# Kernel optimization log

Hardware: AMD Instinct MI355X
Metric: run time of the kernel (lower is better)

The kernel has to match this reference:

```python
import jax, jax.numpy as jnp
import numpy as np

NUM_COMPONENTS = 4
HEADS = 16

def setup_inputs() -> dict:
    key = jax.random.key(0)
    ks = jax.random.split(key, 7)
    BC, S, D = 8, 4096, 1024   # batch*components, latent tokens, hidden dim
    E = 160                     # encoder (text) sequence length
    w_scale = 0.02              # keep logits in a sane range
    return {
        "hidden_states": jax.random.normal(ks[0], (BC, S, D), jnp.float32),
        "encoder_hidden_states": jax.random.normal(ks[1], (BC, E, D), jnp.float32),
        "Wq": jax.random.normal(ks[2], (D, D), jnp.float32) * w_scale,
        "Wk": jax.random.normal(ks[3], (D, D), jnp.float32) * w_scale,
        "Wv": jax.random.normal(ks[4], (D, D), jnp.float32) * w_scale,
        "Wo": jax.random.normal(ks[5], (D, D), jnp.float32) * w_scale,
        "bo": jnp.zeros((D,), jnp.float32),
    }

def reference(hidden_states, encoder_hidden_states, Wq, Wk, Wv, Wo, bo):
    BC, S, D = hidden_states.shape
    E = encoder_hidden_states.shape[1]
    C = NUM_COMPONENTS
    B = BC // C
    H = HEADS
    dh = D // H
    scale = dh ** -0.5

    # projections (diffusers to_q/to_k/to_v, no bias)
    q = hidden_states @ Wq            # [BC, S, D]
    k = encoder_hidden_states @ Wk    # [BC, E, D]
    v = encoder_hidden_states @ Wv    # [BC, E, D]

    q = q.reshape(BC, S, H, dh).transpose(0, 2, 1, 3)  # [BC, H, S, dh]
    k = k.reshape(BC, E, H, dh).transpose(0, 2, 1, 3)  # [BC, H, E, dh]
    v = v.reshape(BC, E, H, dh).transpose(0, 2, 1, 3)  # [BC, H, E, dh]

    scores = jnp.einsum("bhsd,bhtd->bhst", q, k) * scale  # [BC, H, S, E]
    scores_c = scores.reshape(C, B, H, S, E)

    # pooled (mean over encoder tokens) softmax across components
    pooled = scores_c.mean(axis=-1, keepdims=True)         # [C, B, H, S, 1]
    weights_pooled = jax.nn.softmax(pooled, axis=0)        # softmax over components
    # per-row softmax over encoder tokens, scaled by component weight
    weights = jax.nn.softmax(scores_c, axis=-1) * weights_pooled
    weights = weights.reshape(BC, H, S, E)

    out = jnp.einsum("bhst,bhtd->bhsd", weights, v)        # [BC, H, S, dh]
    out = out.transpose(0, 2, 1, 3).reshape(BC, S, D)

    out = out @ Wo + bo        # to_out[0]; to_out[1] is dropout (identity, eval)
    out = out + hidden_states  # residual_connection=True, rescale factor 1
    return out
```

## Files before the change

### kernel.cpp

```cpp
#include <hip/hip_runtime.h>
#include <stdint.h>

typedef __attribute__((ext_vector_type(8))) short short8;
typedef __attribute__((ext_vector_type(4))) float f32x4;
typedef __attribute__((ext_vector_type(4))) unsigned short us4;

#define DI __device__ __forceinline__

static constexpr int Dm = 1024;
static constexpr int Sm = 4096;
static constexpr int Em = 160;
static constexpr int Hm = 16;

static constexpr size_t OFF_HSB  = 0;
static constexpr size_t OFF_WT   = 67108864;
static constexpr size_t OFF_QB   = 75497472;
static constexpr size_t OFF_KB   = 142606336;
static constexpr size_t OFF_VB   = 145227776;
static constexpr size_t OFF_VT   = 147849216;
static constexpr size_t OFF_EHSB = 150994944;

DI unsigned short f2b(float f) {
  union { float f; unsigned u; } x; x.f = f;
  unsigned r = x.u + 0x7fffu + ((x.u >> 16) & 1u);
  return (unsigned short)(r >> 16);
}

DI void gl_lds16(const void* g, void* l) {
  __builtin_amdgcn_global_load_lds(
      (const __attribute__((address_space(1))) unsigned int*)g,
      (__attribute__((address_space(3))) unsigned int*)l, 16, 0, 0);
}

__global__ void k_cvt(const float* __restrict__ in, unsigned short* __restrict__ out, int n4) {
  int stride = gridDim.x * blockDim.x;
  for (int i = blockIdx.x * blockDim.x + threadIdx.x; i < n4; i += stride) {
    float4 v = ((const float4*)in)[i];
    us4 o = { f2b(v.x), f2b(v.y), f2b(v.z), f2b(v.w) };
    *(us4*)(out + (size_t)i * 4) = o;
  }
}

__global__ void k_wtrans(const float* __restrict__ W0, const float* __restrict__ W1,
                         const float* __restrict__ W2, const float* __restrict__ W3,
                         unsigned short* __restrict__ Wt) {
  __shared__ float t[32][33];
  const float* W = (blockIdx.z == 0) ? W0 : (blockIdx.z == 1) ? W1 : (blockIdx.z == 2) ? W2 : W3;
  unsigned short* o = Wt + (size_t)blockIdx.z * 1048576;
  int tx = threadIdx.x, ty = threadIdx.y;
  int n = blockIdx.x * 32 + tx;
  int k0 = blockIdx.y * 32;
  #pragma unroll
  for (int j = ty; j < 32; j += 8) t[j][tx] = W[(size_t)(k0 + j) * 1024 + n];
  __syncthreads();
  #pragma unroll
  for (int j = ty; j < 32; j += 8)
    o[(size_t)(blockIdx.x * 32 + j) * 1024 + k0 + tx] = f2b(t[tx][j]);
}

template<int MODE>
__global__ __launch_bounds__(256, 2) void k_gemm(const unsigned short* __restrict__ A,
                                                 const unsigned short* __restrict__ Bt,
                                                 void* __restrict__ Cout,
                                                 const float* __restrict__ bias,
                                                 const float* __restrict__ resid) {
  __shared__ __align__(16) char smem[32768];
  char* As = smem;
  char* Bs = smem + 16384;
  const int tid = threadIdx.x;
  const int lane = tid & 63;
  const int l15 = lane & 15;
  const int g = lane >> 4;
  const int wv = tid >> 6;
  const int wr = wv >> 1, wc = wv & 1;
  const int m0 = blockIdx.x * 128, n0 = blockIdx.y * 128;

  f32x4 acc[4][4];
  #pragma unroll
  for (int i = 0; i < 4; ++i)
    #pragma unroll
    for (int j = 0; j < 4; ++j) acc[i][j] = (f32x4){0.f, 0.f, 0.f, 0.f};

  for (int t = 0; t < 16; ++t) {
    __syncthreads();
    #pragma unroll
    for (int is = 0; is < 4; ++is) {
      int ch = is * 256 + tid;
      int row = ch >> 3, j = ch & 7;
      int sj = (j ^ (row & 7)) * 8;
      gl_lds16(A  + (size_t)(m0 + row) * 1024 + t * 64 + sj, As + ch * 16);
      gl_lds16(Bt + (size_t)(n0 + row) * 1024 + t * 64 + sj, Bs + ch * 16);
    }
    __syncthreads();
    short8 af[2][4], bf[2][4];
    #pragma unroll
    for (int kk = 0; kk < 2; ++kk)
      #pragma unroll
      for (int mt = 0; mt < 4; ++mt) {
        af[kk][mt] = *(const short8*)(As + (wr * 64 + mt * 16 + l15) * 128 + ((kk * 64 + g * 16) ^ ((l15 & 7) << 4)));
        bf[kk][mt] = *(const short8*)(Bs + (wc * 64 + mt * 16 + l15) * 128 + ((kk * 64 + g * 16) ^ ((l15 & 7) << 4)));
      }
    #pragma unroll
    for (int kk = 0; kk < 2; ++kk)
      #pragma unroll
      for (int mt = 0; mt < 4; ++mt)
        #pragma unroll
        for (int nt = 0; nt < 4; ++nt)
          acc[mt][nt] = __builtin_amdgcn_mfma_f32_16x16x32_bf16(af[kk][mt], bf[kk][nt], acc[mt][nt], 0, 0, 0);
  }

  #pragma unroll
  for (int mt = 0; mt < 4; ++mt)
    #pragma unroll
    for (int nt = 0; nt < 4; ++nt)
      #pragma unroll
      for (int r = 0; r < 4; ++r) {
        size_t row = (size_t)(m0 + wr * 64 + mt * 16 + 4 * g + r);
        int col = n0 + wc * 64 + nt * 16 + l15;
        size_t idx = row * 1024 + col;
        if (MODE == 0) ((unsigned short*)Cout)[idx] = f2b(acc[mt][nt][r]);
        else           ((float*)Cout)[idx] = acc[mt][nt][r] + bias[col] + resid[idx];
      }
}

__global__ __launch_bounds__(256, 2) void k_gemm_kv(const unsigned short* __restrict__ A,
                                                    const unsigned short* __restrict__ Wt,
                                                    unsigned short* __restrict__ kb,
                                                    unsigned short* __restrict__ vt) {
  __shared__ __align__(16) char smem[32768];
  char* As = smem;
  char* Bs = smem + 16384;
  const int tid = threadIdx.x;
  const int lane = tid & 63;
  const int l15 = lane & 15;
  const int g = lane >> 4;
  const int wv = tid >> 6;
  const int wr = wv >> 1, wc = wv & 1;
  const int m0 = blockIdx.x * 128, n0 = blockIdx.y * 128;
  const int z = blockIdx.z;
  const unsigned short* Bt = Wt + (size_t)(1 + z) * 1048576;

  f32x4 acc[4][4];
  #pragma unroll
  for (int i = 0; i < 4; ++i)
    #pragma unroll
    for (int j = 0; j < 4; ++j) acc[i][j] = (f32x4){0.f, 0.f, 0.f, 0.f};

  for (int t = 0; t < 16; ++t) {
    __syncthreads();
    #pragma unroll
    for (int is = 0; is < 4; ++is) {
      int ch = is * 256 + tid;
      int row = ch >> 3, j = ch & 7;
      int sj = (j ^ (row & 7)) * 8;
      gl_lds16(A  + (size_t)(m0 + row) * 1024 + t * 64 + sj, As + ch * 16);
      gl_lds16(Bt + (size_t)(n0 + row) * 1024 + t * 64 + sj, Bs + ch * 16);
    }
    __syncthreads();
    short8 af[2][4], bf[2][4];
    #pragma unroll
    for (int kk = 0; kk < 2; ++kk)
      #pragma unroll
      for (int mt = 0; mt < 4; ++mt) {
        af[kk][mt] = *(const short8*)(As + (wr * 64 + mt * 16 + l15) * 128 + ((kk * 64 + g * 16) ^ ((l15 & 7) << 4)));
        bf[kk][mt] = *(const short8*)(Bs + (wc * 64 + mt * 16 + l15) * 128 + ((kk * 64 + g * 16) ^ ((l15 & 7) << 4)));
      }
    #pragma unroll
    for (int kk = 0; kk < 2; ++kk)
      #pragma unroll
      for (int mt = 0; mt < 4; ++mt)
        #pragma unroll
        for (int nt = 0; nt < 4; ++nt)
          acc[mt][nt] = __builtin_amdgcn_mfma_f32_16x16x32_bf16(af[kk][mt], bf[kk][nt], acc[mt][nt], 0, 0, 0);
  }

  #pragma unroll
  for (int mt = 0; mt < 4; ++mt)
    #pragma unroll
    for (int nt = 0; nt < 4; ++nt)
      #pragma unroll
      for (int r = 0; r < 4; ++r) {
        int row = m0 + wr * 64 + mt * 16 + 4 * g + r;
        int col = n0 + wc * 64 + nt * 16 + l15;
        unsigned short hv = f2b(acc[mt][nt][r]);
        if (z == 0) {
          kb[(size_t)row * 1024 + col] = hv;
        } else {
          int bc = row / 160, e = row - bc * 160;
          vt[((size_t)(bc * 16 + (col >> 6)) * 64 + (col & 63)) * 192 + e] = hv;
        }
      }
}

__global__ __launch_bounds__(256, 2) void k_attn(const unsigned short* __restrict__ Qb,
                                                 const unsigned short* __restrict__ Kb,
                                                 const unsigned short* __restrict__ Vt,
                                                 unsigned short* __restrict__ AOb) {
  __shared__ __align__(16) char smem[22528];
  float* pooled = (float*)(smem + 21504);
  const int tid = threadIdx.x, lane = tid & 63, wv = tid >> 6;
  const int g = lane >> 4, l15 = lane & 15;
  const int s0 = blockIdx.x * 64;
  const int h = blockIdx.y;
  const int b = blockIdx.z;
  const int bc = wv * 2 + b;
  const float scale = 0.125f;

  const unsigned short* Qp = Qb + ((size_t)bc * Sm + s0) * Dm + h * 64;
  const unsigned short* Kp = Kb + (size_t)bc * Em * Dm + h * 64;
  const unsigned short* Vp = Vt + ((size_t)bc * Hm + h) * (64 * 192);
  unsigned short* Op = AOb + ((size_t)bc * Sm + s0) * Dm + h * 64;
  char* Pw = smem + wv * 5376;

  #pragma unroll 1
  for (int st = 0; st < 4; ++st) {
    short8 qf[2];
    #pragma unroll
    for (int kk = 0; kk < 2; ++kk)
      qf[kk] = *(const short8*)(Qp + (size_t)(st * 16 + l15) * Dm + kk * 32 + g * 8);
    f32x4 sc[10];
    #pragma unroll
    for (int et = 0; et < 10; ++et) {
      sc[et] = (f32x4){0.f, 0.f, 0.f, 0.f};
      #pragma unroll
      for (int kk = 0; kk < 2; ++kk) {
        short8 kf = *(const short8*)(Kp + (size_t)(et * 16 + l15) * Dm + kk * 32 + g * 8);
        sc[et] = __builtin_amdgcn_mfma_f32_16x16x32_bf16(qf[kk], kf, sc[et], 0, 0, 0);
      }
    }
    float rs4[4];
    #pragma unroll
    for (int r = 0; r < 4; ++r) {
      float v = 0.f;
      #pragma unroll
      for (int et = 0; et < 10; ++et) v += sc[et][r];
      v += __shfl_xor(v, 1); v += __shfl_xor(v, 2); v += __shfl_xor(v, 4); v += __shfl_xor(v, 8);
      if (l15 == 0) pooled[(st * 16 + 4 * g + r) * 4 + wv] = v * (scale / 160.f);
      float mx = sc[0][r];
      #pragma unroll
      for (int et = 1; et < 10; ++et) mx = fmaxf(mx, sc[et][r]);
      mx = fmaxf(mx, __shfl_xor(mx, 1)); mx = fmaxf(mx, __shfl_xor(mx, 2));
      mx = fmaxf(mx, __shfl_xor(mx, 4)); mx = fmaxf(mx, __shfl_xor(mx, 8));
      float rs = 0.f;
      #pragma unroll
      for (int et = 0; et < 10; ++et) {
        float p = __expf((sc[et][r] - mx) * scale);
        rs += p;
        *(unsigned short*)(Pw + (4 * g + r) * 336 + (et * 16 + l15) * 2) = f2b(p);
      }
      rs += __shfl_xor(rs, 1); rs += __shfl_xor(rs, 2); rs += __shfl_xor(rs, 4); rs += __shfl_xor(rs, 8);
      rs4[r] = rs;
    }
    f32x4 oa[4];
    #pragma unroll
    for (int dt = 0; dt < 4; ++dt) oa[dt] = (f32x4){0.f, 0.f, 0.f, 0.f};
    #pragma unroll
    for (int k5 = 0; k5 < 5; ++k5) {
      short8 pf = *(const short8*)(Pw + l15 * 336 + k5 * 64 + g * 16);
      #pragma unroll
      for (int dt = 0; dt < 4; ++dt) {
        short8 vf = *(const short8*)(Vp + (size_t)(dt * 16 + l15) * 192 + k5 * 32 + g * 8);
        oa[dt] = __builtin_amdgcn_mfma_f32_16x16x32_bf16(pf, vf, oa[dt], 0, 0, 0);
      }
    }
    __syncthreads();
    #pragma unroll
    for (int r = 0; r < 4; ++r) {
      float4 pl = *(const float4*)&pooled[(st * 16 + 4 * g + r) * 4];
      float m3 = fmaxf(fmaxf(pl.x, pl.y), fmaxf(pl.z, pl.w));
      float ssum = __expf(pl.x - m3) + __expf(pl.y - m3) + __expf(pl.z - m3) + __expf(pl.w - m3);
      float mine = (wv == 0) ? pl.x : (wv == 1) ? pl.y : (wv == 2) ? pl.z : pl.w;
      float srw = __expf(mine - m3) / (ssum * rs4[r]);
      #pragma unroll
      for (int dt = 0; dt < 4; ++dt)
        Op[(size_t)(st * 16 + 4 * g + r) * Dm + dt * 16 + l15] = f2b(oa[dt][r] * srw);
    }
  }
}

extern "C" void kernel_launch(void* const* d_in, const int* in_sizes, int n_in,
                              void* d_out, int out_size, void* d_ws, size_t ws_size,
                              hipStream_t stream) {
  const float* hs  = (const float*)d_in[0];
  const float* ehs = (const float*)d_in[1];
  const float* Wq  = (const float*)d_in[2];
  const float* Wk  = (const float*)d_in[3];
  const float* Wv  = (const float*)d_in[4];
  const float* Wo  = (const float*)d_in[5];
  const float* bo  = (const float*)d_in[6];
  char* ws = (char*)d_ws;
  unsigned short* hsb = (unsigned short*)(ws + OFF_HSB);
  unsigned short* wt  = (unsigned short*)(ws + OFF_WT);
  unsigned short* qb  = (unsigned short*)(ws + OFF_QB);
  unsigned short* kb  = (unsigned short*)(ws + OFF_KB);
  unsigned short* vt  = (unsigned short*)(ws + OFF_VT);
  unsigned short* eb  = (unsigned short*)(ws + OFF_EHSB);

  hipLaunchKernelGGL(k_cvt, dim3(2048), dim3(256), 0, stream, hs, hsb, 8 * 4096 * 1024 / 4);
  hipLaunchKernelGGL(k_cvt, dim3(1280), dim3(256), 0, stream, ehs, eb, 8 * 160 * 1024 / 4);
  hipLaunchKernelGGL(k_wtrans, dim3(32, 32, 4), dim3(32, 8), 0, stream, Wq, Wk, Wv, Wo, wt);
  hipLaunchKernelGGL((k_gemm<0>), dim3(256, 8), dim3(256), 0, stream, hsb, wt, (void*)qb,
                     (const float*)nullptr, (const float*)nullptr);
  hipLaunchKernelGGL(k_gemm_kv, dim3(10, 8, 2), dim3(256), 0, stream, eb, wt, kb, vt);
  hipLaunchKernelGGL(k_attn, dim3(64, 16, 2), dim3(256), 0, stream, qb, kb, vt, hsb);
  hipLaunchKernelGGL((k_gemm<1>), dim3(256, 8), dim3(256), 0, stream, hsb, wt + 3 * 1048576, d_out, bo, hs);
}
```

Measured before the change: 359.8 us.

## Fuse fp32-to-bf16 conversion of hidden states into Q GEMM and swizzle block order

Drops the standalone conversion kernel for the 128MB fp32 hidden states and converts A tiles to bf16 inside the Q projection GEMM, writing them to LDS with regular loads and stores. This removes a full write and reread of the bf16 copy. Both GEMMs also switch to a 1D grid with grouped tile ordering, so blocks that share B tiles and A rows run close together for better L2 reuse. The cost is synchronous fp32 loads and per-element conversion inside the GEMM mainloop instead of async global-to-LDS loads.

```diff
diff --git a/kernel.cpp b/kernel.cpp
--- a/kernel.cpp
+++ b/kernel.cpp
@@ -16,7 +16,6 @@
 static constexpr size_t OFF_WT   = 67108864;
 static constexpr size_t OFF_QB   = 75497472;
 static constexpr size_t OFF_KB   = 142606336;
-static constexpr size_t OFF_VB   = 145227776;
 static constexpr size_t OFF_VT   = 147849216;
 static constexpr size_t OFF_EHSB = 150994944;
 
@@ -58,8 +57,8 @@
     o[(size_t)(blockIdx.x * 32 + j) * 1024 + k0 + tx] = f2b(t[tx][j]);
 }
 
-template<int MODE>
-__global__ __launch_bounds__(256, 2) void k_gemm(const unsigned short* __restrict__ A,
+template<int MODE, int CVTA>
+__global__ __launch_bounds__(256, 2) void k_gemm(const void* __restrict__ Ain,
                                                  const unsigned short* __restrict__ Bt,
                                                  void* __restrict__ Cout,
                                                  const float* __restrict__ bias,
@@ -73,7 +72,9 @@
   const int g = lane >> 4;
   const int wv = tid >> 6;
   const int wr = wv >> 1, wc = wv & 1;
-  const int m0 = blockIdx.x * 128, n0 = blockIdx.y * 128;
+  const int bid = blockIdx.x;
+  const int m0 = ((bid >> 6) * 8 + (bid & 7)) * 128;
+  const int n0 = ((bid >> 3) & 7) * 128;
 
   f32x4 acc[4][4];
   #pragma unroll
@@ -88,8 +89,23 @@
       int ch = is * 256 + tid;
       int row = ch >> 3, j = ch & 7;
       int sj = (j ^ (row & 7)) * 8;
-      gl_lds16(A  + (size_t)(m0 + row) * 1024 + t * 64 + sj, As + ch * 16);
       gl_lds16(Bt + (size_t)(n0 + row) * 1024 + t * 64 + sj, Bs + ch * 16);
+      if constexpr (!CVTA)
+        gl_lds16((const unsigned short*)Ain + (size_t)(m0 + row) * 1024 + t * 64 + sj, As + ch * 16);
+    }
+    if constexpr (CVTA) {
+      #pragma unroll
+      for (int is = 0; is < 4; ++is) {
+        int ch = is * 256 + tid;
+        int row = ch >> 3, j = ch & 7;
+        int sj = (j ^ (row & 7)) * 8;
+        const float* src = (const float*)Ain + (size_t)(m0 + row) * 1024 + t * 64 + sj;
+        float4 v0 = *(const float4*)src;
+        float4 v1 = *(const float4*)(src + 4);
+        short8 o = { (short)f2b(v0.x), (short)f2b(v0.y), (short)f2b(v0.z), (short)f2b(v0.w),
+                     (short)f2b(v1.x), (short)f2b(v1.y), (short)f2b(v1.z), (short)f2b(v1.w) };
+        *(short8*)(As + ch * 16) = o;
+      }
     }
     __syncthreads();
     short8 af[2][4], bf[2][4];
@@ -296,12 +312,11 @@
   unsigned short* vt  = (unsigned short*)(ws + OFF_VT);
   unsigned short* eb  = (unsigned short*)(ws + OFF_EHSB);
 
-  hipLaunchKernelGGL(k_cvt, dim3(2048), dim3(256), 0, stream, hs, hsb, 8 * 4096 * 1024 / 4);
   hipLaunchKernelGGL(k_cvt, dim3(1280), dim3(256), 0, stream, ehs, eb, 8 * 160 * 1024 / 4);
   hipLaunchKernelGGL(k_wtrans, dim3(32, 32, 4), dim3(32, 8), 0, stream, Wq, Wk, Wv, Wo, wt);
-  hipLaunchKernelGGL((k_gemm<0>), dim3(256, 8), dim3(256), 0, stream, hsb, wt, (void*)qb,
+  hipLaunchKernelGGL((k_gemm<0, 1>), dim3(2048), dim3(256), 0, stream, (const void*)hs, wt, (void*)qb,
                      (const float*)nullptr, (const float*)nullptr);
   hipLaunchKernelGGL(k_gemm_kv, dim3(10, 8, 2), dim3(256), 0, stream, eb, wt, kb, vt);
   hipLaunchKernelGGL(k_attn, dim3(64, 16, 2), dim3(256), 0, stream, qb, kb, vt, hsb);
-  hipLaunchKernelGGL((k_gemm<1>), dim3(256, 8), dim3(256), 0, stream, hsb, wt + 3 * 1048576, d_out, bo, hs);
-}
+  hipLaunchKernelGGL((k_gemm<1, 0>), dim3(2048), dim3(256), 0, stream, (const void*)hsb, wt + 3 * 1048576, d_out, bo, hs);
+}
```

New measurement: 358.1 us. About the same (-0.5%).

## Use 256x256 double-buffered GEMM tiles with grouped block order for Q and output projections

Applied to the files above, without the earlier changes.

Replaces the 128x128 single-buffered GEMM with a 512-thread 256x256 tile kernel. The next K-slice is prefetched into a second LDS buffer while the current one is consumed, and MFMA phases are raised in priority. Blocks are remapped so that groups of M tiles share N tiles, improving L2 reuse. Larger tiles raise arithmetic intensity and halve the global loads per FLOP, but the kernel uses 128KB of LDS, which limits occupancy to one block per CU. Launch order is also shuffled so the KV projection runs before the hidden-state conversion.

```diff
diff --git a/kernel.cpp b/kernel.cpp
--- a/kernel.cpp
+++ b/kernel.cpp
@@ -16,7 +16,6 @@
 static constexpr size_t OFF_WT   = 67108864;
 static constexpr size_t OFF_QB   = 75497472;
 static constexpr size_t OFF_KB   = 142606336;
-static constexpr size_t OFF_VB   = 145227776;
 static constexpr size_t OFF_VT   = 147849216;
 static constexpr size_t OFF_EHSB = 150994944;
 
@@ -59,67 +58,90 @@
 }
 
 template<int MODE>
-__global__ __launch_bounds__(256, 2) void k_gemm(const unsigned short* __restrict__ A,
-                                                 const unsigned short* __restrict__ Bt,
-                                                 void* __restrict__ Cout,
-                                                 const float* __restrict__ bias,
-                                                 const float* __restrict__ resid) {
-  __shared__ __align__(16) char smem[32768];
-  char* As = smem;
-  char* Bs = smem + 16384;
+__global__ __launch_bounds__(512, 2) void k_gemm256(const unsigned short* __restrict__ A,
+                                                    const unsigned short* __restrict__ Bt,
+                                                    void* __restrict__ Cout,
+                                                    const float* __restrict__ bias,
+                                                    const float* __restrict__ resid) {
+  __shared__ __align__(16) char smem[131072];
   const int tid = threadIdx.x;
   const int lane = tid & 63;
   const int l15 = lane & 15;
   const int g = lane >> 4;
   const int wv = tid >> 6;
-  const int wr = wv >> 1, wc = wv & 1;
-  const int m0 = blockIdx.x * 128, n0 = blockIdx.y * 128;
-
-  f32x4 acc[4][4];
-  #pragma unroll
-  for (int i = 0; i < 4; ++i)
+  const int wr = wv >> 2;
+  const int wcn = wv & 3;
+  const int bid = blockIdx.x;
+  const int m0 = (((bid >> 5) << 3) + (bid & 7)) * 256;
+  const int n0 = ((bid >> 3) & 3) * 256;
+
+  f32x4 acc[8][4];
+  #pragma unroll
+  for (int i = 0; i < 8; ++i)
     #pragma unroll
     for (int j = 0; j < 4; ++j) acc[i][j] = (f32x4){0.f, 0.f, 0.f, 0.f};
 
+  auto STAGE = [&](int bb, int t) {
+    #pragma unroll
+    for (int ps = 0; ps < 4; ++ps) {
+      int ch = ps * 512 + tid;
+      int row = ch >> 3, j = ch & 7;
+      int sj = (j ^ (row & 7)) * 8;
+      gl_lds16(A  + (size_t)(m0 + row) * 1024 + t * 64 + sj, smem + bb * 32768 + ch * 16);
+      gl_lds16(Bt + (size_t)(n0 + row) * 1024 + t * 64 + sj, smem + 65536 + bb * 32768 + ch * 16);
+    }
+  };
+
+  STAGE(0, 0);
+  int cb = 0;
   for (int t = 0; t < 16; ++t) {
     __syncthreads();
-    #pragma unroll
-    for (int is = 0; is < 4; ++is) {
-      int ch = is * 256 + tid;
-      int row = ch >> 3, j = ch & 7;
-      int sj = (j ^ (row & 7)) * 8;
-      gl_lds16(A  + (size_t)(m0 + row) * 1024 + t * 64 + sj, As + ch * 16);
-      gl_lds16(Bt + (size_t)(n0 + row) * 1024 + t * 64 + sj, Bs + ch * 16);
-    }
-    __syncthreads();
-    short8 af[2][4], bf[2][4];
-    #pragma unroll
-    for (int kk = 0; kk < 2; ++kk)
-      #pragma unroll
-      for (int mt = 0; mt < 4; ++mt) {
-        af[kk][mt] = *(const short8*)(As + (wr * 64 + mt * 16 + l15) * 128 + ((kk * 64 + g * 16) ^ ((l15 & 7) << 4)));
-        bf[kk][mt] = *(const short8*)(Bs + (wc * 64 + mt * 16 + l15) * 128 + ((kk * 64 + g * 16) ^ ((l15 & 7) << 4)));
-      }
-    #pragma unroll
-    for (int kk = 0; kk < 2; ++kk)
-      #pragma unroll
-      for (int mt = 0; mt < 4; ++mt)
+    if (t < 15) STAGE(cb ^ 1, t + 1);
+    const char* Ab = smem + cb * 32768;
+    const char* Bb = smem + 65536 + cb * 32768;
+    #pragma unroll
+    for (int ph = 0; ph < 4; ++ph) {
+      const int mh = ph >> 1;
+      const int nh = (ph >> 1) ^ (ph & 1);
+      short8 af[2][4], bf[2][2];
+      #pragma unroll
+      for (int kk = 0; kk < 2; ++kk) {
         #pragma unroll
-        for (int nt = 0; nt < 4; ++nt)
-          acc[mt][nt] = __builtin_amdgcn_mfma_f32_16x16x32_bf16(af[kk][mt], bf[kk][nt], acc[mt][nt], 0, 0, 0);
+        for (int mt = 0; mt < 4; ++mt)
+          af[kk][mt] = *(const short8*)(Ab + (wr * 128 + mh * 64 + mt * 16 + l15) * 128 +
+                                        ((kk * 64 + g * 16) ^ ((l15 & 7) << 4)));
+        #pragma unroll
+        for (int nt = 0; nt < 2; ++nt)
+          bf[kk][nt] = *(const short8*)(Bb + (wcn * 64 + nh * 32 + nt * 16 + l15) * 128 +
+                                        ((kk * 64 + g * 16) ^ ((l15 & 7) << 4)));
+      }
+      __builtin_amdgcn_sched_barrier(0);
+      __builtin_amdgcn_s_setprio(1);
+      #pragma unroll
+      for (int kk = 0; kk < 2; ++kk)
+        #pragma unroll
+        for (int mt = 0; mt < 4; ++mt)
+          #pragma unroll
+          for (int nt = 0; nt < 2; ++nt)
+            acc[mh * 4 + mt][nh * 2 + nt] = __builtin_amdgcn_mfma_f32_16x16x32_bf16(
+                af[kk][mt], bf[kk][nt], acc[mh * 4 + mt][nh * 2 + nt], 0, 0, 0);
+      __builtin_amdgcn_s_setprio(0);
+      __builtin_amdgcn_sched_barrier(0);
+    }
+    cb ^= 1;
   }
 
   #pragma unroll
-  for (int mt = 0; mt < 4; ++mt)
-    #pragma unroll
-    for (int nt = 0; nt < 4; ++nt)
+  for (int m = 0; m < 8; ++m)
+    #pragma unroll
+    for (int n = 0; n < 4; ++n)
       #pragma unroll
       for (int r = 0; r < 4; ++r) {
-        size_t row = (size_t)(m0 + wr * 64 + mt * 16 + 4 * g + r);
-        int col = n0 + wc * 64 + nt * 16 + l15;
+        size_t row = (size_t)(m0 + wr * 128 + m * 16 + 4 * g + r);
+        int col = n0 + wcn * 64 + n * 16 + l15;
         size_t idx = row * 1024 + col;
-        if (MODE == 0) ((unsigned short*)Cout)[idx] = f2b(acc[mt][nt][r]);
-        else           ((float*)Cout)[idx] = acc[mt][nt][r] + bias[col] + resid[idx];
+        if (MODE == 0) ((unsigned short*)Cout)[idx] = f2b(acc[m][n][r]);
+        else           ((float*)Cout)[idx] = acc[m][n][r] + bias[col] + resid[idx];
       }
 }
 
@@ -296,12 +318,12 @@
   unsigned short* vt  = (unsigned short*)(ws + OFF_VT);
   unsigned short* eb  = (unsigned short*)(ws + OFF_EHSB);
 
-  hipLaunchKernelGGL(k_cvt, dim3(2048), dim3(256), 0, stream, hs, hsb, 8 * 4096 * 1024 / 4);
   hipLaunchKernelGGL(k_cvt, dim3(1280), dim3(256), 0, stream, ehs, eb, 8 * 160 * 1024 / 4);
   hipLaunchKernelGGL(k_wtrans, dim3(32, 32, 4), dim3(32, 8), 0, stream, Wq, Wk, Wv, Wo, wt);
-  hipLaunchKernelGGL((k_gemm<0>), dim3(256, 8), dim3(256), 0, stream, hsb, wt, (void*)qb,
+  hipLaunchKernelGGL(k_gemm_kv, dim3(10, 8, 2), dim3(256), 0, stream, eb, wt, kb, vt);
+  hipLaunchKernelGGL(k_cvt, dim3(2048), dim3(256), 0, stream, hs, hsb, 8 * 4096 * 1024 / 4);
+  hipLaunchKernelGGL((k_gemm256<0>), dim3(512), dim3(512), 0, stream, hsb, wt, (void*)qb,
                      (const float*)nullptr, (const float*)nullptr);
-  hipLaunchKernelGGL(k_gemm_kv, dim3(10, 8, 2), dim3(256), 0, stream, eb, wt, kb, vt);
   hipLaunchKernelGGL(k_attn, dim3(64, 16, 2), dim3(256), 0, stream, qb, kb, vt, hsb);
-  hipLaunchKernelGGL((k_gemm<1>), dim3(256, 8), dim3(256), 0, stream, hsb, wt + 3 * 1048576, d_out, bo, hs);
-}
+  hipLaunchKernelGGL((k_gemm256<1>), dim3(512), dim3(512), 0, stream, hsb, wt + 3 * 1048576, d_out, bo, hs);
+}
```

After: 351.9 us. 1.02x faster.

## Merge prep kernels, co-schedule KV GEMM with hs conversion, swizzle GEMM tiles

Applied to the files above, without the earlier changes.

The ehs conversion and weight transpose now share one launch. A second launch runs the K/V projection GEMM blocks alongside the hidden-state bf16 conversion blocks. The Q and output GEMMs use a 1D grid with block swizzling for L2 reuse, and the Q GEMM stages its bf16 results through LDS so global stores are 16-byte and coalesced. The goal is fewer kernel launches and less idle time between them, plus better store efficiency, at the cost of more branching inside kernels and uneven block workloads.

```diff
diff --git a/kernel.cpp b/kernel.cpp
--- a/kernel.cpp
+++ b/kernel.cpp
@@ -16,7 +16,6 @@
 static constexpr size_t OFF_WT   = 67108864;
 static constexpr size_t OFF_QB   = 75497472;
 static constexpr size_t OFF_KB   = 142606336;
-static constexpr size_t OFF_VB   = 145227776;
 static constexpr size_t OFF_VT   = 147849216;
 static constexpr size_t OFF_EHSB = 150994944;
 
@@ -32,48 +31,59 @@
       (__attribute__((address_space(3))) unsigned int*)l, 16, 0, 0);
 }
 
-__global__ void k_cvt(const float* __restrict__ in, unsigned short* __restrict__ out, int n4) {
-  int stride = gridDim.x * blockDim.x;
-  for (int i = blockIdx.x * blockDim.x + threadIdx.x; i < n4; i += stride) {
-    float4 v = ((const float4*)in)[i];
+__global__ void k_prep0(const float* __restrict__ ehs, unsigned short* __restrict__ eb,
+                        const float* __restrict__ W0, const float* __restrict__ W1,
+                        const float* __restrict__ W2, const float* __restrict__ W3,
+                        unsigned short* __restrict__ Wt) {
+  __shared__ float t[32][33];
+  const int bid = blockIdx.x, tid = threadIdx.x;
+  if (bid < 4096) {
+    const int bz = bid >> 10, rest = bid & 1023, by = rest >> 5, bx = rest & 31;
+    const float* W = (bz == 0) ? W0 : (bz == 1) ? W1 : (bz == 2) ? W2 : W3;
+    unsigned short* o = Wt + (size_t)bz * 1048576;
+    const int tx = tid & 31, ty = tid >> 5;
+    const int n = bx * 32 + tx, k0 = by * 32;
+    #pragma unroll
+    for (int j = ty; j < 32; j += 8) t[j][tx] = W[(size_t)(k0 + j) * 1024 + n];
+    __syncthreads();
+    #pragma unroll
+    for (int j = ty; j < 32; j += 8)
+      o[(size_t)(bx * 32 + j) * 1024 + k0 + tx] = f2b(t[tx][j]);
+  } else {
+    const int i = (bid - 4096) * 256 + tid;
+    float4 v = ((const float4*)ehs)[i];
     us4 o = { f2b(v.x), f2b(v.y), f2b(v.z), f2b(v.w) };
-    *(us4*)(out + (size_t)i * 4) = o;
-  }
-}
-
-__global__ void k_wtrans(const float* __restrict__ W0, const float* __restrict__ W1,
-                         const float* __restrict__ W2, const float* __restrict__ W3,
-                         unsigned short* __restrict__ Wt) {
-  __shared__ float t[32][33];
-  const float* W = (blockIdx.z == 0) ? W0 : (blockIdx.z == 1) ? W1 : (blockIdx.z == 2) ? W2 : W3;
-  unsigned short* o = Wt + (size_t)blockIdx.z * 1048576;
-  int tx = threadIdx.x, ty = threadIdx.y;
-  int n = blockIdx.x * 32 + tx;
-  int k0 = blockIdx.y * 32;
-  #pragma unroll
-  for (int j = ty; j < 32; j += 8) t[j][tx] = W[(size_t)(k0 + j) * 1024 + n];
-  __syncthreads();
-  #pragma unroll
-  for (int j = ty; j < 32; j += 8)
-    o[(size_t)(blockIdx.x * 32 + j) * 1024 + k0 + tx] = f2b(t[tx][j]);
-}
-
-template<int MODE>
-__global__ __launch_bounds__(256, 2) void k_gemm(const unsigned short* __restrict__ A,
-                                                 const unsigned short* __restrict__ Bt,
-                                                 void* __restrict__ Cout,
-                                                 const float* __restrict__ bias,
-                                                 const float* __restrict__ resid) {
+    *(us4*)(eb + (size_t)i * 4) = o;
+  }
+}
+
+__global__ __launch_bounds__(256, 2) void k_prep1(const float* __restrict__ hs,
+                                                  unsigned short* __restrict__ hsb,
+                                                  const unsigned short* __restrict__ eb,
+                                                  const unsigned short* __restrict__ Wt,
+                                                  unsigned short* __restrict__ kb,
+                                                  unsigned short* __restrict__ vt) {
   __shared__ __align__(16) char smem[32768];
+  const int bid = blockIdx.x, tid = threadIdx.x;
+  if (bid >= 160) {
+    const int stride = 2048 * 256;
+    for (int i = (bid - 160) * 256 + tid; i < 8388608; i += stride) {
+      float4 v = ((const float4*)hs)[i];
+      us4 o = { f2b(v.x), f2b(v.y), f2b(v.z), f2b(v.w) };
+      *(us4*)(hsb + (size_t)i * 4) = o;
+    }
+    return;
+  }
   char* As = smem;
   char* Bs = smem + 16384;
-  const int tid = threadIdx.x;
   const int lane = tid & 63;
   const int l15 = lane & 15;
   const int g = lane >> 4;
   const int wv = tid >> 6;
   const int wr = wv >> 1, wc = wv & 1;
-  const int m0 = blockIdx.x * 128, n0 = blockIdx.y * 128;
+  const int z = bid / 80, rr = bid - z * 80;
+  const int m0 = (rr % 10) * 128, n0 = (rr / 10) * 128;
+  const unsigned short* Bt = Wt + (size_t)(1 + z) * 1048576;
 
   f32x4 acc[4][4];
   #pragma unroll
@@ -88,72 +98,7 @@
       int ch = is * 256 + tid;
       int row = ch >> 3, j = ch & 7;
       int sj = (j ^ (row & 7)) * 8;
-      gl_lds16(A  + (size_t)(m0 + row) * 1024 + t * 64 + sj, As + ch * 16);
-      gl_lds16(Bt + (size_t)(n0 + row) * 1024 + t * 64 + sj, Bs + ch * 16);
-    }
-    __syncthreads();
-    short8 af[2][4], bf[2][4];
-    #pragma unroll
-    for (int kk = 0; kk < 2; ++kk)
-      #pragma unroll
-      for (int mt = 0; mt < 4; ++mt) {
-        af[kk][mt] = *(const short8*)(As + (wr * 64 + mt * 16 + l15) * 128 + ((kk * 64 + g * 16) ^ ((l15 & 7) << 4)));
-        bf[kk][mt] = *(const short8*)(Bs + (wc * 64 + mt * 16 + l15) * 128 + ((kk * 64 + g * 16) ^ ((l15 & 7) << 4)));
-      }
-    #pragma unroll
-    for (int kk = 0; kk < 2; ++kk)
-      #pragma unroll
-      for (int mt = 0; mt < 4; ++mt)
-        #pragma unroll
-        for (int nt = 0; nt < 4; ++nt)
-          acc[mt][nt] = __builtin_amdgcn_mfma_f32_16x16x32_bf16(af[kk][mt], bf[kk][nt], acc[mt][nt], 0, 0, 0);
-  }
-
-  #pragma unroll
-  for (int mt = 0; mt < 4; ++mt)
-    #pragma unroll
-    for (int nt = 0; nt < 4; ++nt)
-      #pragma unroll
-      for (int r = 0; r < 4; ++r) {
-        size_t row = (size_t)(m0 + wr * 64 + mt * 16 + 4 * g + r);
-        int col = n0 + wc * 64 + nt * 16 + l15;
-        size_t idx = row * 1024 + col;
-        if (MODE == 0) ((unsigned short*)Cout)[idx] = f2b(acc[mt][nt][r]);
-        else           ((float*)Cout)[idx] = acc[mt][nt][r] + bias[col] + resid[idx];
-      }
-}
-
-__global__ __launch_bounds__(256, 2) void k_gemm_kv(const unsigned short* __restrict__ A,
-                                                    const unsigned short* __restrict__ Wt,
-                                                    unsigned short* __restrict__ kb,
-                                                    unsigned short* __restrict__ vt) {
-  __shared__ __align__(16) char smem[32768];
-  char* As = smem;
-  char* Bs = smem + 16384;
-  const int tid = threadIdx.x;
-  const int lane = tid & 63;
-  const int l15 = lane & 15;
-  const int g = lane >> 4;
-  const int wv = tid >> 6;
-  const int wr = wv >> 1, wc = wv & 1;
-  const int m0 = blockIdx.x * 128, n0 = blockIdx.y * 128;
-  const int z = blockIdx.z;
-  const unsigned short* Bt = Wt + (size_t)(1 + z) * 1048576;
-
-  f32x4 acc[4][4];
-  #pragma unroll
-  for (int i = 0; i < 4; ++i)
-    #pragma unroll
-    for (int j = 0; j < 4; ++j) acc[i][j] = (f32x4){0.f, 0.f, 0.f, 0.f};
-
-  for (int t = 0; t < 16; ++t) {
-    __syncthreads();
-    #pragma unroll
-    for (int is = 0; is < 4; ++is) {
-      int ch = is * 256 + tid;
-      int row = ch >> 3, j = ch & 7;
-      int sj = (j ^ (row & 7)) * 8;
-      gl_lds16(A  + (size_t)(m0 + row) * 1024 + t * 64 + sj, As + ch * 16);
+      gl_lds16(eb + (size_t)(m0 + row) * 1024 + t * 64 + sj, As + ch * 16);
       gl_lds16(Bt + (size_t)(n0 + row) * 1024 + t * 64 + sj, Bs + ch * 16);
     }
     __syncthreads();
@@ -190,6 +135,92 @@
           vt[((size_t)(bc * 16 + (col >> 6)) * 64 + (col & 63)) * 192 + e] = hv;
         }
       }
+}
+
+template<int MODE>
+__global__ __launch_bounds__(256, 2) void k_gemm128(const unsigned short* __restrict__ A,
+                                                    const unsigned short* __restrict__ Bt,
+                                                    void* __restrict__ Cout,
+                                                    const float* __restrict__ bias,
+                                                    const float* __restrict__ resid) {
+  __shared__ __align__(16) char smem[32768];
+  char* As = smem;
+  char* Bs = smem + 16384;
+  const int tid = threadIdx.x;
+  const int lane = tid & 63;
+  const int l15 = lane & 15;
+  const int g = lane >> 4;
+  const int wv = tid >> 6;
+  const int wr = wv >> 1, wc = wv & 1;
+  const int bid = blockIdx.x;
+  const int m0 = ((bid >> 6) * 8 + (bid & 7)) * 128;
+  const int n0 = ((bid >> 3) & 7) * 128;
+
+  f32x4 acc[4][4];
+  #pragma unroll
+  for (int i = 0; i < 4; ++i)
+    #pragma unroll
+    for (int j = 0; j < 4; ++j) acc[i][j] = (f32x4){0.f, 0.f, 0.f, 0.f};
+
+  for (int t = 0; t < 16; ++t) {
+    __syncthreads();
+    #pragma unroll
+    for (int is = 0; is < 4; ++is) {
+      int ch = is * 256 + tid;
+      int row = ch >> 3, j = ch & 7;
+      int sj = (j ^ (row & 7)) * 8;
+      gl_lds16(A  + (size_t)(m0 + row) * 1024 + t * 64 + sj, As + ch * 16);
+      gl_lds16(Bt + (size_t)(n0 + row) * 1024 + t * 64 + sj, Bs + ch * 16);
+    }
+    __syncthreads();
+    short8 af[2][4], bf[2][4];
+    #pragma unroll
+    for (int kk = 0; kk < 2; ++kk)
+      #pragma unroll
+      for (int mt = 0; mt < 4; ++mt) {
+        af[kk][mt] = *(const short8*)(As + (wr * 64 + mt * 16 + l15) * 128 + ((kk * 64 + g * 16) ^ ((l15 & 7) << 4)));
+        bf[kk][mt] = *(const short8*)(Bs + (wc * 64 + mt * 16 + l15) * 128 + ((kk * 64 + g * 16) ^ ((l15 & 7) << 4)));
+      }
+    #pragma unroll
+    for (int kk = 0; kk < 2; ++kk)
+      #pragma unroll
+      for (int mt = 0; mt < 4; ++mt)
+        #pragma unroll
+        for (int nt = 0; nt < 4; ++nt)
+          acc[mt][nt] = __builtin_amdgcn_mfma_f32_16x16x32_bf16(af[kk][mt], bf[kk][nt], acc[mt][nt], 0, 0, 0);
+  }
+
+  if (MODE == 0) {
+    __syncthreads();
+    unsigned short* Cl = (unsigned short*)smem;
+    #pragma unroll
+    for (int mt = 0; mt < 4; ++mt)
+      #pragma unroll
+      for (int nt = 0; nt < 4; ++nt)
+        #pragma unroll
+        for (int r = 0; r < 4; ++r)
+          Cl[(wr * 64 + mt * 16 + 4 * g + r) * 128 + wc * 64 + nt * 16 + l15] = f2b(acc[mt][nt][r]);
+    __syncthreads();
+    #pragma unroll
+    for (int j = 0; j < 8; ++j) {
+      int ch = j * 256 + tid;
+      int row = ch >> 4, sl = ch & 15;
+      *(short8*)((unsigned short*)Cout + (size_t)(m0 + row) * 1024 + n0 + sl * 8) =
+          *(const short8*)(Cl + row * 128 + sl * 8);
+    }
+  } else {
+    #pragma unroll
+    for (int mt = 0; mt < 4; ++mt)
+      #pragma unroll
+      for (int nt = 0; nt < 4; ++nt)
+        #pragma unroll
+        for (int r = 0; r < 4; ++r) {
+          size_t row = (size_t)(m0 + wr * 64 + mt * 16 + 4 * g + r);
+          int col = n0 + wc * 64 + nt * 16 + l15;
+          size_t idx = row * 1024 + col;
+          ((float*)Cout)[idx] = acc[mt][nt][r] + bias[col] + resid[idx];
+        }
+  }
 }
 
 __global__ __launch_bounds__(256, 2) void k_attn(const unsigned short* __restrict__ Qb,
@@ -296,12 +327,10 @@
   unsigned short* vt  = (unsigned short*)(ws + OFF_VT);
   unsigned short* eb  = (unsigned short*)(ws + OFF_EHSB);
 
-  hipLaunchKernelGGL(k_cvt, dim3(2048), dim3(256), 0, stream, hs, hsb, 8 * 4096 * 1024 / 4);
-  hipLaunchKernelGGL(k_cvt, dim3(1280), dim3(256), 0, stream, ehs, eb, 8 * 160 * 1024 / 4);
-  hipLaunchKernelGGL(k_wtrans, dim3(32, 32, 4), dim3(32, 8), 0, stream, Wq, Wk, Wv, Wo, wt);
-  hipLaunchKernelGGL((k_gemm<0>), dim3(256, 8), dim3(256), 0, stream, hsb, wt, (void*)qb,
+  hipLaunchKernelGGL(k_prep0, dim3(4096 + 1280), dim3(256), 0, stream, ehs, eb, Wq, Wk, Wv, Wo, wt);
+  hipLaunchKernelGGL(k_prep1, dim3(160 + 2048), dim3(256), 0, stream, hs, hsb, eb, wt, kb, vt);
+  hipLaunchKernelGGL((k_gemm128<0>), dim3(2048), dim3(256), 0, stream, hsb, wt, (void*)qb,
                      (const float*)nullptr, (const float*)nullptr);
-  hipLaunchKernelGGL(k_gemm_kv, dim3(10, 8, 2), dim3(256), 0, stream, eb, wt, kb, vt);
   hipLaunchKernelGGL(k_attn, dim3(64, 16, 2), dim3(256), 0, stream, qb, kb, vt, hsb);
-  hipLaunchKernelGGL((k_gemm<1>), dim3(256, 8), dim3(256), 0, stream, hsb, wt + 3 * 1048576, d_out, bo, hs);
-}
+  hipLaunchKernelGGL((k_gemm128<1>), dim3(2048), dim3(256), 0, stream, hsb, wt + 3 * 1048576, d_out, bo, hs);
+}
```

Result: faster. 327.9 us (-8.9%).
